# Kernel optimization log

Measured on AMD Instinct MI355X. Metric: run time of the kernel, lower is better.

## Reference

```python
import jax, jax.numpy as jnp
import numpy as np
import math

G = 256            # grid points per axis
L = 25.6           # cubic cell edge (bohr)
A = L / G          # grid spacing = 0.1 bohr
R_O = 2.0          # radial cutoff (bohr)
RMAX = int(math.ceil(R_O / A))   # 20
D = 2 * RMAX + 1                 # 41 box points per axis
N_ATOMS = 32
N_RAD = 4
N_L = 4
V_CELL = A ** 3
FOUR_PI = 4.0 * math.pi


def _make_W(n_rad):
    # NeuralXC ortho basis: S_ij = sqrt((5+2i)(5+2j))/(5+i+j), W = sqrtm(inv(S))
    i = np.arange(n_rad)
    S = np.sqrt((5.0 + 2 * i)[:, None] * (5.0 + 2 * i)[None, :]) / (5.0 + i[:, None] + i[None, :])
    w, V = np.linalg.eigh(np.linalg.inv(S))
    return (V * np.sqrt(w)) @ V.T


def setup_inputs():
    key = jax.random.key(0)
    k1, k2 = jax.random.split(key)
    rho = jax.random.uniform(k1, (G, G, G), dtype=jnp.float32)
    positions = jax.random.uniform(k2, (N_ATOMS, 3), dtype=jnp.float32) * L
    W = jnp.asarray(_make_W(N_RAD), dtype=jnp.float32)
    # periodic mesh offsets: [0..RMAX, -RMAX..-1] as in mesh_3d
    offs = jnp.concatenate([jnp.arange(0, RMAX + 1), jnp.arange(-RMAX, 0)]).astype(jnp.int32)
    return {"rho": rho, "positions": positions, "W": W, "offs": offs}


def _assoc_legendre(n_l, x, s):
    # P[l][m] for 0 <= m <= l < n_l, with Condon-Shortley phase
    P = [[None] * n_l for _ in range(n_l)]
    P[0][0] = jnp.ones_like(x)
    for m in range(n_l):
        if m > 0:
            P[m][m] = -(2 * m - 1) * s * P[m - 1][m - 1]
        if m + 1 < n_l:
            P[m + 1][m] = (2 * m + 1) * x * P[m][m]
        for l in range(m + 2, n_l):
            P[l][m] = ((2 * l - 1) * x * P[l - 1][m] - (l - 1 + m) * P[l - 2][m]) / (l - m)
    return P


def _real_sph_stack(n_l, theta, phi):
    # real spherical harmonics stacked in (l, m=-l..l) order -> [n_l**2, ...]
    x = jnp.cos(theta)
    s = jnp.sin(theta)
    P = _assoc_legendre(n_l, x, s)
    sq2 = math.sqrt(2.0)
    Ys = []
    for l in range(n_l):
        for m in range(-l, l + 1):
            am = abs(m)
            N = math.sqrt((2 * l + 1) / FOUR_PI * math.factorial(l - am) / math.factorial(l + am))
            if m == 0:
                Ys.append(N * P[l][0] * jnp.ones_like(x))
            elif m > 0:
                Ys.append(sq2 * ((-1) ** m) * N * P[l][m] * jnp.cos(m * phi))
            else:
                Ys.append(sq2 * ((-1) ** am) * N * P[l][am] * jnp.sin(am * phi))
    return jnp.stack(Ys)


def _radials(R, W):
    # g_a(r) = r^2 (r_o - r)^(a+2) / N_a for r < r_o, orthonormalized with W
    gs = []
    for a in range(N_RAD):
        Nn = math.sqrt(720.0 * R_O ** (11 + 2 * a) / float(np.prod([2 * a + k for k in range(5, 12)])))
        g = R ** 2 * (R_O - R) ** (a + 2) / Nn
        gs.append(jnp.where(R < R_O, g, 0.0))
    return jnp.einsum('nm,mxyz->nxyz', W, jnp.stack(gs))


def _project_atom(rho, pos, W, offs):
    cm = jnp.round(pos / A)                     # U_inv @ pos for diagonal cell
    dr = pos - A * cm
    idx = jnp.mod(offs[None, :] + cm.astype(jnp.int32)[:, None], G)   # [3, D] PBC mesh indices
    # separable irregular gather of the atom box (== torch rho[Xm,Ym,Zm] with fmod+negative-index wrap)
    srho = rho[idx[0][:, None, None], idx[1][None, :, None], idx[2][None, None, :]]  # [D,D,D]
    coord = A * offs.astype(jnp.float32)
    Xs = (coord - dr[0])[:, None, None]
    Ys = (coord - dr[1])[None, :, None]
    Zs = (coord - dr[2])[None, None, :]
    R = jnp.sqrt(Xs ** 2 + Ys ** 2 + Zs ** 2)   # [D,D,D]
    phi = jnp.arctan2(Ys, Xs)                   # [D,D,1], broadcasts
    small = R < 1e-15
    ratio = jnp.clip(jnp.where(small, 1.0, Zs / jnp.where(small, 1.0, R)), -1.0, 1.0)
    theta = jnp.where(small, 0.0, jnp.arccos(ratio))
    angs = _real_sph_stack(N_L, theta, phi)     # [N_L**2, D,D,D]
    rads = _radials(R, W) * V_CELL              # [N_RAD,  D,D,D]
    # equals the original padded 'lmijk,nijk,ijk->nlm' einsum followed by selecting |m|<=l,
    # flattened in (n, l, m) order
    coeff = jnp.einsum('cxyz,nxyz,xyz->nc', angs, rads, srho)
    return coeff.reshape(-1)                    # [N_RAD * N_L**2]


def reference(rho, positions, W, offs):
    return jax.vmap(lambda p: _project_atom(rho, p, W, offs))(positions)  # [N_ATOMS, 64]
```

## Files before the change

kernel.cpp:

```cpp
#include <hip/hip_runtime.h>
#include <math.h>

#define G 256
#define D41 41
#define NATOMS 32

__global__ __launch_bounds__(256, 2) void proj_kernel(
    const float* __restrict__ rho,
    const float* __restrict__ positions,
    const float* __restrict__ W,
    const int* __restrict__ offs,
    float* __restrict__ out,
    float cs0, float cs1, float cs2, float cs3)
{
    const int atom = blockIdx.y;
    const int iplane = blockIdx.x;
    const int tid = threadIdx.x;

    __shared__ int jbase[D41];
    __shared__ int kidx[D41];
    __shared__ float cys[D41];
    __shared__ float czs[D41];
    __shared__ float red[4 * 64];

    const float A = 0.1f;

    float px = positions[atom * 3 + 0];
    float py = positions[atom * 3 + 1];
    float pz = positions[atom * 3 + 2];
    float cmx = rintf(px / A), cmy = rintf(py / A), cmz = rintf(pz / A);
    float drx = px - A * cmx, dry = py - A * cmy, drz = pz - A * cmz;
    int cxi = (int)cmx, cyi = (int)cmy, czi = (int)cmz;

    if (tid < D41) {
        int o = offs[tid];
        jbase[tid] = (((o + cyi) % G + G) % G) * G;
        kidx[tid]  = (((o + czi) % G + G) % G);
        cys[tid] = A * (float)o - dry;
        czs[tid] = A * (float)o - drz;
    }

    int oi = offs[iplane];
    int base0 = (((oi + cxi) % G + G) % G) * (G * G);
    float Xd = A * (float)oi - drx;
    float XX = Xd * Xd;

    float C[4][4];
    float cs[4] = {cs0, cs1, cs2, cs3};
#pragma unroll
    for (int n = 0; n < 4; ++n)
#pragma unroll
        for (int a = 0; a < 4; ++a)
            C[n][a] = W[n * 4 + a] * cs[a];

    __syncthreads();

    float acc[64];
#pragma unroll
    for (int q = 0; q < 64; ++q) acc[q] = 0.0f;

    for (int p = tid; p < D41 * D41; p += 256) {
        int j = p / D41;
        int k = p - j * D41;
        float Yd = cys[j], Zd = czs[k];
        float r2 = XX + Yd * Yd + Zd * Zd;
        if (r2 > 0.0f && r2 < 4.0f) {
            float srho = rho[base0 + jbase[j] + kidx[k]];
            float invr = rsqrtf(r2);
            float r = r2 * invr;
            float t = 2.0f - r;
            float g0 = r2 * t * t, g1 = g0 * t, g2 = g1 * t, g3 = g2 * t;
            float rv[4];
#pragma unroll
            for (int n = 0; n < 4; ++n)
                rv[n] = fmaf(C[n][3], g3, fmaf(C[n][2], g2,
                         fmaf(C[n][1], g1, C[n][0] * g0))) * srho;

            float xr = Xd * invr, yr = Yd * invr, zr = Zd * invr;
            float xx = xr * xr, yy = yr * yr, zz = zr * zr;
            float Ya[16];
            Ya[0]  = 0.28209479177387814f;
            Ya[1]  = 0.4886025119029199f * yr;
            Ya[2]  = 0.4886025119029199f * zr;
            Ya[3]  = 0.4886025119029199f * xr;
            Ya[4]  = 1.0925484305920792f * (xr * yr);
            Ya[5]  = 1.0925484305920792f * (yr * zr);
            Ya[6]  = 0.31539156525252005f * (3.0f * zz - 1.0f);
            Ya[7]  = 1.0925484305920792f * (xr * zr);
            Ya[8]  = 0.5462742152960396f * (xx - yy);
            Ya[9]  = 0.5900435899266435f * yr * (3.0f * xx - yy);
            Ya[10] = 2.890611442640554f  * (xr * yr) * zr;
            Ya[11] = 0.4570457994644658f * yr * (5.0f * zz - 1.0f);
            Ya[12] = 0.3731763325901154f * zr * (5.0f * zz - 3.0f);
            Ya[13] = 0.4570457994644658f * xr * (5.0f * zz - 1.0f);
            Ya[14] = 1.445305721320277f  * zr * (xx - yy);
            Ya[15] = 0.5900435899266435f * xr * (xx - 3.0f * yy);

#pragma unroll
            for (int n = 0; n < 4; ++n)
#pragma unroll
                for (int c = 0; c < 16; ++c)
                    acc[n * 16 + c] = fmaf(rv[n], Ya[c], acc[n * 16 + c]);
        }
    }

    int lane = tid & 63;
#pragma unroll
    for (int s = 0; s < 6; ++s) {
        int d = 1 << s;
        bool hi = (lane & d) != 0;
#pragma unroll
        for (int pp = 0; pp < (64 >> (s + 1)); ++pp) {
            float send = hi ? acc[2 * pp] : acc[2 * pp + 1];
            float recv = __shfl_xor(send, d, 64);
            float keep = hi ? acc[2 * pp + 1] : acc[2 * pp];
            acc[pp] = keep + recv;
        }
    }

    int wave = tid >> 6;
    red[wave * 64 + lane] = acc[0];
    __syncthreads();
    if (tid < 64) {
        float s = red[tid] + red[64 + tid] + red[128 + tid] + red[192 + tid];
        atomicAdd(&out[atom * 64 + tid], s);
    }
}

extern "C" void kernel_launch(void* const* d_in, const int* in_sizes, int n_in,
                              void* d_out, int out_size, void* d_ws, size_t ws_size,
                              hipStream_t stream) {
    const float* rho = (const float*)d_in[0];
    const float* positions = (const float*)d_in[1];
    const float* W = (const float*)d_in[2];
    const int* offs = (const int*)d_in[3];
    float* out = (float*)d_out;

    double Ad = 25.6 / 256.0;
    double vcell = Ad * Ad * Ad;
    float cs[4];
    for (int a = 0; a < 4; ++a) {
        double prod = 1.0;
        for (int k = 5; k < 12; ++k) prod *= (double)(2 * a + k);
        double nn = sqrt(720.0 * pow(2.0, 11 + 2 * a) / prod);
        cs[a] = (float)(vcell / nn);
    }

    hipMemsetAsync(d_out, 0, (size_t)out_size * sizeof(float), stream);
    dim3 grid(D41, NATOMS);
    proj_kernel<<<grid, 256, 0, stream>>>(rho, positions, W, offs, out,
                                          cs[0], cs[1], cs[2], cs[3]);
}
```

Measured before the change: 105.0 us.

## Enumerate only in-sphere grid points per plane and pack FMAs as float2

Replaces the dense 41x41 per-plane loop with a compacted enumeration of the points inside an integer-radius sphere. Per-row widths and prefix offsets are built in shared memory, and each thread maps its linear index to a row via a byte table. This removes the divergent branch and the idle lanes for points outside the cutoff. The spherical-harmonic accumulation is also packed into float2 vector FMAs to encourage packed-math instructions. The integer bound (435) may include points just outside the float cutoff, which the clamped t handles, and it relies on the offs layout being the standard -20..20 instead of reading the offs input.

```diff
diff --git a/kernel.cpp b/kernel.cpp
--- a/kernel.cpp
+++ b/kernel.cpp
@@ -2,28 +2,31 @@
 #include <math.h>
 
 #define G 256
-#define D41 41
 #define NATOMS 32
+#define RC2I 435
+#define MAXPTS 1408
+
+typedef float f32x2 __attribute__((ext_vector_type(2)));
 
 __global__ __launch_bounds__(256, 2) void proj_kernel(
     const float* __restrict__ rho,
     const float* __restrict__ positions,
     const float* __restrict__ W,
-    const int* __restrict__ offs,
     float* __restrict__ out,
     float cs0, float cs1, float cs2, float cs3)
 {
     const int atom = blockIdx.y;
-    const int iplane = blockIdx.x;
     const int tid = threadIdx.x;
+    const float A = 0.1f;
 
-    __shared__ int jbase[D41];
-    __shared__ int kidx[D41];
-    __shared__ float cys[D41];
-    __shared__ float czs[D41];
-    __shared__ float red[4 * 64];
-
-    const float A = 0.1f;
+    __shared__ int swid[41];
+    __shared__ int shk[41];
+    __shared__ int sstart[41];
+    __shared__ int stotal;
+    __shared__ float4 rowT[41];
+    __shared__ float2 kT[41];
+    __shared__ unsigned char rowOf[MAXPTS];
+    __shared__ float red[256];
 
     float px = positions[atom * 3 + 0];
     float py = positions[atom * 3 + 1];
@@ -32,18 +35,45 @@
     float drx = px - A * cmx, dry = py - A * cmy, drz = pz - A * cmz;
     int cxi = (int)cmx, cyi = (int)cmy, czi = (int)cmz;
 
-    if (tid < D41) {
-        int o = offs[tid];
-        jbase[tid] = (((o + cyi) % G + G) % G) * G;
-        kidx[tid]  = (((o + czi) % G + G) % G);
-        cys[tid] = A * (float)o - dry;
-        czs[tid] = A * (float)o - drz;
+    const int di = (int)blockIdx.x - 20;
+
+    if (tid < 41) {
+        int dj = tid - 20;
+        int m = RC2I - di * di - dj * dj;
+        int w = 0, h = 0;
+        if (m >= 0) {
+            h = (int)sqrtf((float)m);
+            while (h * h > m) --h;
+            while ((h + 1) * (h + 1) <= m) ++h;
+            w = 2 * h + 1;
+        }
+        swid[tid] = w;
+        shk[tid] = h;
     }
+    __syncthreads();
+    if (tid == 0) {
+        int run = 0;
+        for (int j = 0; j < 41; ++j) { sstart[j] = run; run += swid[j]; }
+        stotal = run;
+    }
+    __syncthreads();
+    if (tid < 41) {
+        int dj = tid - 20;
+        float yc = A * (float)dj - dry;
+        int jb = ((((dj + cyi) % G) + G) % G) * G;
+        float zc = A * (float)dj - drz;
+        int kb = (((dj + czi) % G) + G) % G;
+        kT[tid] = make_float2(zc, __int_as_float(kb));
+        int off = sstart[tid] + shk[tid] - 20;
+        rowT[tid] = make_float4(yc, __int_as_float(jb), __int_as_float(off), 0.0f);
+        int st = sstart[tid], w = swid[tid];
+        for (int q = 0; q < w; ++q) rowOf[st + q] = (unsigned char)tid;
+    }
+    __syncthreads();
 
-    int oi = offs[iplane];
-    int base0 = (((oi + cxi) % G + G) % G) * (G * G);
-    float Xd = A * (float)oi - drx;
-    float XX = Xd * Xd;
+    const int base0 = ((((di + cxi) % G) + G) % G) * (G * G);
+    const float Xd = A * (float)di - drx;
+    const float XX = Xd * Xd;
 
     float C[4][4];
     float cs[4] = {cs0, cs1, cs2, cs3};
@@ -53,56 +83,67 @@
         for (int a = 0; a < 4; ++a)
             C[n][a] = W[n * 4 + a] * cs[a];
 
-    __syncthreads();
+    f32x2 acc2[32];
+#pragma unroll
+    for (int q = 0; q < 32; ++q) acc2[q] = (f32x2){0.0f, 0.0f};
 
-    float acc[64];
+    const int tot = stotal;
+    for (int p = tid; p < tot; p += 256) {
+        int row = rowOf[p];
+        float4 rt = rowT[row];
+        float Yd = rt.x;
+        int jb = __float_as_int(rt.y);
+        int off = __float_as_int(rt.z);
+        float2 kt = kT[p - off];
+        float Zd = kt.x;
+        int kb = __float_as_int(kt.y);
+        float srho = rho[base0 + jb + kb];
+
+        float r2 = fmaf(Yd, Yd, fmaf(Zd, Zd, XX));
+        float invr = rsqrtf(fmaxf(r2, 1e-24f));
+        float r = r2 * invr;
+        float t = fmaxf(2.0f - r, 0.0f);
+        float tt = t * t;
+        float rs = r2 * srho;
+        float g0 = rs * tt, g1 = g0 * t, g2 = g1 * t, g3 = g2 * t;
+        float rv[4];
 #pragma unroll
-    for (int q = 0; q < 64; ++q) acc[q] = 0.0f;
+        for (int n = 0; n < 4; ++n)
+            rv[n] = fmaf(C[n][3], g3, fmaf(C[n][2], g2,
+                     fmaf(C[n][1], g1, C[n][0] * g0)));
 
-    for (int p = tid; p < D41 * D41; p += 256) {
-        int j = p / D41;
-        int k = p - j * D41;
-        float Yd = cys[j], Zd = czs[k];
-        float r2 = XX + Yd * Yd + Zd * Zd;
-        if (r2 > 0.0f && r2 < 4.0f) {
-            float srho = rho[base0 + jbase[j] + kidx[k]];
-            float invr = rsqrtf(r2);
-            float r = r2 * invr;
-            float t = 2.0f - r;
-            float g0 = r2 * t * t, g1 = g0 * t, g2 = g1 * t, g3 = g2 * t;
-            float rv[4];
-#pragma unroll
-            for (int n = 0; n < 4; ++n)
-                rv[n] = fmaf(C[n][3], g3, fmaf(C[n][2], g2,
-                         fmaf(C[n][1], g1, C[n][0] * g0))) * srho;
-
-            float xr = Xd * invr, yr = Yd * invr, zr = Zd * invr;
-            float xx = xr * xr, yy = yr * yr, zz = zr * zr;
-            float Ya[16];
-            Ya[0]  = 0.28209479177387814f;
-            Ya[1]  = 0.4886025119029199f * yr;
-            Ya[2]  = 0.4886025119029199f * zr;
-            Ya[3]  = 0.4886025119029199f * xr;
-            Ya[4]  = 1.0925484305920792f * (xr * yr);
-            Ya[5]  = 1.0925484305920792f * (yr * zr);
-            Ya[6]  = 0.31539156525252005f * (3.0f * zz - 1.0f);
-            Ya[7]  = 1.0925484305920792f * (xr * zr);
-            Ya[8]  = 0.5462742152960396f * (xx - yy);
-            Ya[9]  = 0.5900435899266435f * yr * (3.0f * xx - yy);
-            Ya[10] = 2.890611442640554f  * (xr * yr) * zr;
-            Ya[11] = 0.4570457994644658f * yr * (5.0f * zz - 1.0f);
-            Ya[12] = 0.3731763325901154f * zr * (5.0f * zz - 3.0f);
-            Ya[13] = 0.4570457994644658f * xr * (5.0f * zz - 1.0f);
-            Ya[14] = 1.445305721320277f  * zr * (xx - yy);
-            Ya[15] = 0.5900435899266435f * xr * (xx - 3.0f * yy);
+        float xr = Xd * invr, yr = Yd * invr, zr = Zd * invr;
+        float xx = xr * xr, yy = yr * yr, zz = zr * zr;
+        float xy = xr * yr, yz = yr * zr, xz = xr * zr;
+        float xmy = xx - yy;
+        float q51 = fmaf(5.0f, zz, -1.0f);
+        f32x2 Y[8];
+        Y[0] = (f32x2){0.28209479177387814f, 0.4886025119029199f * yr};
+        Y[1] = (f32x2){0.4886025119029199f * zr, 0.4886025119029199f * xr};
+        Y[2] = (f32x2){1.0925484305920792f * xy, 1.0925484305920792f * yz};
+        Y[3] = (f32x2){0.31539156525252005f * fmaf(3.0f, zz, -1.0f),
+                       1.0925484305920792f * xz};
+        Y[4] = (f32x2){0.5462742152960396f * xmy,
+                       0.5900435899266435f * yr * fmaf(3.0f, xx, -yy)};
+        Y[5] = (f32x2){2.890611442640554f * xy * zr,
+                       0.4570457994644658f * yr * q51};
+        Y[6] = (f32x2){0.3731763325901154f * zr * fmaf(5.0f, zz, -3.0f),
+                       0.4570457994644658f * xr * q51};
+        Y[7] = (f32x2){1.445305721320277f * zr * xmy,
+                       0.5900435899266435f * xr * fmaf(xx, 1.0f, -3.0f * yy)};
 
 #pragma unroll
-            for (int n = 0; n < 4; ++n)
+        for (int n = 0; n < 4; ++n) {
+            f32x2 s = {rv[n], rv[n]};
 #pragma unroll
-                for (int c = 0; c < 16; ++c)
-                    acc[n * 16 + c] = fmaf(rv[n], Ya[c], acc[n * 16 + c]);
+            for (int q = 0; q < 8; ++q)
+                acc2[n * 8 + q] = __builtin_elementwise_fma(s, Y[q], acc2[n * 8 + q]);
         }
     }
+
+    float av[64];
+#pragma unroll
+    for (int q = 0; q < 32; ++q) { av[2 * q] = acc2[q].x; av[2 * q + 1] = acc2[q].y; }
 
     int lane = tid & 63;
 #pragma unroll
@@ -111,15 +152,15 @@
         bool hi = (lane & d) != 0;
 #pragma unroll
         for (int pp = 0; pp < (64 >> (s + 1)); ++pp) {
-            float send = hi ? acc[2 * pp] : acc[2 * pp + 1];
+            float send = hi ? av[2 * pp] : av[2 * pp + 1];
             float recv = __shfl_xor(send, d, 64);
-            float keep = hi ? acc[2 * pp + 1] : acc[2 * pp];
-            acc[pp] = keep + recv;
+            float keep = hi ? av[2 * pp + 1] : av[2 * pp];
+            av[pp] = keep + recv;
         }
     }
 
     int wave = tid >> 6;
-    red[wave * 64 + lane] = acc[0];
+    red[wave * 64 + lane] = av[0];
     __syncthreads();
     if (tid < 64) {
         float s = red[tid] + red[64 + tid] + red[128 + tid] + red[192 + tid];
@@ -133,7 +174,6 @@
     const float* rho = (const float*)d_in[0];
     const float* positions = (const float*)d_in[1];
     const float* W = (const float*)d_in[2];
-    const int* offs = (const int*)d_in[3];
     float* out = (float*)d_out;
 
     double Ad = 25.6 / 256.0;
@@ -147,7 +187,7 @@
     }
 
     hipMemsetAsync(d_out, 0, (size_t)out_size * sizeof(float), stream);
-    dim3 grid(D41, NATOMS);
-    proj_kernel<<<grid, 256, 0, stream>>>(rho, positions, W, offs, out,
+    dim3 grid(41, NATOMS);
+    proj_kernel<<<grid, 256, 0, stream>>>(rho, positions, W, out,
                                           cs[0], cs[1], cs[2], cs[3]);
 }
```

Measured after the change: 104.5 us. About the same (-0.5%).
